# Kernel optimization log

Hardware: AMD Instinct MI355X
Metric: run time of the kernel (lower is better)

The kernel has to match this reference:

```python
import jax, jax.numpy as jnp
import numpy as np

N = 100000        # nodes
E_RAND = 1500000  # random edges (self loops appended -> E = 1.6M)
IN_DIM = 500
HID = 256
NCLASS = 50
K = 10


def setup_inputs() -> dict:
    key = jax.random.key(0)
    ks = jax.random.split(key, 8)
    feats = jax.random.normal(ks[0], (N, IN_DIM), dtype=jnp.float32)
    # edges: random + self loops (fit() adds self loops)
    src_r = jax.random.randint(ks[1], (E_RAND,), 0, N, dtype=jnp.int32)
    dst_r = jax.random.randint(ks[2], (E_RAND,), 0, N, dtype=jnp.int32)
    loop = jnp.arange(N, dtype=jnp.int32)
    src = jnp.concatenate([src_r, loop])
    dst = jnp.concatenate([dst_r, loop])
    # params (xavier-uniform-like scales)
    def xavier(k, shape):
        lim = np.sqrt(6.0 / (shape[0] + shape[1]))
        return jax.random.uniform(k, shape, jnp.float32, -lim, lim)
    W1 = xavier(ks[3], (IN_DIM, HID))
    b1 = jnp.zeros((HID,), jnp.float32)
    W2 = xavier(ks[4], (HID, NCLASS))
    b2 = jnp.zeros((NCLASS,), jnp.float32)
    s = xavier(ks[5], (NCLASS, 1))
    return {"feats": feats, "W1": W1, "b1": b1, "W2": W2, "b2": b2,
            "s": s, "src": src, "dst": dst}


def reference(feats, W1, b1, W2, b2, s, src, dst):
    # --- MLP (dropout is identity in eval / p=0) ---
    x = jax.nn.relu(feats @ W1 + b1)          # [N, HID]
    x = x @ W2 + b2                            # [N, NCLASS]
    # --- DAGNNConv: k-hop sym-normalized propagation ---
    deg = jax.ops.segment_sum(jnp.ones_like(dst, dtype=jnp.float32), dst,
                              num_segments=N)  # in-degrees
    norm = jnp.power(deg, -0.5)[:, None]       # [N, 1]
    results = [x]
    h = x
    for _ in range(K):
        h = h * norm
        h = jax.ops.segment_sum(h[src], dst, num_segments=N)  # copy_u + sum
        h = h * norm
        results.append(h)
    H = jnp.stack(results, axis=1)             # [N, K+1, C]
    S = jax.nn.sigmoid(jnp.einsum('nkc,co->nk', H, s))  # [N, K+1]
    out = jnp.einsum('nk,nkc->nc', S, H)       # [N, C]
    return out
```

## Files before the change

kernel.cpp:

```cpp
#include <hip/hip_runtime.h>
#include <hip/hip_bf16.h>
#include <math.h>

#define NN     100000
#define INDIM  500
#define HID    256
#define NCLASS 50
#define KHOPS  10
#define KPAD   512
#define CPAD   64

static inline size_t roundup256(size_t x) { return (x + 255) & ~(size_t)255; }

typedef __attribute__((ext_vector_type(8))) short bf16x8;
typedef __attribute__((ext_vector_type(4))) float f32x4;
typedef __attribute__((ext_vector_type(4))) short short4v;

__device__ inline short f2bf(float f) {
    union { float f; unsigned u; } v; v.f = f;
    unsigned r = v.u + 0x7FFFu + ((v.u >> 16) & 1u);
    return (short)(r >> 16);
}
__device__ inline float bflo(unsigned u) {
    union { unsigned u; float f; } v; v.u = u << 16; return v.f;
}
__device__ inline float bfhi(unsigned u) {
    union { unsigned u; float f; } v; v.u = u & 0xFFFF0000u; return v.f;
}
__device__ inline unsigned packbf(float a, float b) {
    return (unsigned)(unsigned short)f2bf(a) | ((unsigned)(unsigned short)f2bf(b) << 16);
}

__global__ void dagnn_zero2(int* __restrict__ a, int* __restrict__ b, int n) {
    int i = blockIdx.x * blockDim.x + threadIdx.x;
    if (i < n) { a[i] = 0; b[i] = 0; }
}

__global__ void dagnn_deg(const int* __restrict__ dst, int* __restrict__ degi, int E) {
    int e = blockIdx.x * blockDim.x + threadIdx.x;
    if (e < E) atomicAdd(&degi[dst[e]], 1);
}

__global__ void dagnn_norm(const int* __restrict__ degi, float* __restrict__ nrm, int n) {
    int i = blockIdx.x * blockDim.x + threadIdx.x;
    if (i < n) nrm[i] = rsqrtf((float)degi[i]);
}

__global__ void dagnn_scan(const int* __restrict__ degi, int* __restrict__ rowptr, int n) {
    __shared__ int wsum[16];
    __shared__ int carry_s;
    const int tid  = threadIdx.x;
    const int lane = tid & 63;
    const int wid  = tid >> 6;
    if (tid == 0) carry_s = 0;
    __syncthreads();
    for (int base = 0; base < n; base += 4096) {
        int i0 = base + tid * 4;
        int v0 = (i0 + 0 < n) ? degi[i0 + 0] : 0;
        int v1 = (i0 + 1 < n) ? degi[i0 + 1] : 0;
        int v2 = (i0 + 2 < n) ? degi[i0 + 2] : 0;
        int v3 = (i0 + 3 < n) ? degi[i0 + 3] : 0;
        int tsum = v0 + v1 + v2 + v3;
        int x = tsum;
        #pragma unroll
        for (int off = 1; off < 64; off <<= 1) {
            int t = __shfl_up(x, off);
            if (lane >= off) x += t;
        }
        if (lane == 63) wsum[wid] = x;
        __syncthreads();
        if (tid == 0) {
            int run = carry_s;
            #pragma unroll
            for (int w = 0; w < 16; ++w) { int t = wsum[w]; wsum[w] = run; run += t; }
            carry_s = run;
        }
        __syncthreads();
        int texcl = wsum[wid] + (x - tsum);
        if (i0 + 0 < n) rowptr[i0 + 0] = texcl;
        if (i0 + 1 < n) rowptr[i0 + 1] = texcl + v0;
        if (i0 + 2 < n) rowptr[i0 + 2] = texcl + v0 + v1;
        if (i0 + 3 < n) rowptr[i0 + 3] = texcl + v0 + v1 + v2;
        __syncthreads();
    }
    if (tid == 0) rowptr[n] = carry_s;
}

__global__ void dagnn_fill(const int* __restrict__ src, const int* __restrict__ dst,
                           const int* __restrict__ rowptr, int* __restrict__ fillc,
                           int* __restrict__ colidx, int E) {
    int e = blockIdx.x * blockDim.x + threadIdx.x;
    if (e >= E) return;
    int d = dst[e];
    int pos = rowptr[d] + atomicAdd(&fillc[d], 1);
    colidx[pos] = src[e];
}

__global__ void dagnn_w1t(const float* __restrict__ W1, short* __restrict__ W1t) {
    int idx = blockIdx.x * 256 + threadIdx.x;
    if (idx >= HID * KPAD) return;
    int n = idx >> 9;
    int k = idx & (KPAD - 1);
    float v = (k < INDIM) ? W1[(size_t)k * HID + n] : 0.f;
    W1t[idx] = f2bf(v);
}

__global__ void dagnn_w2t(const float* __restrict__ W2, short* __restrict__ W2t) {
    int idx = blockIdx.x * 256 + threadIdx.x;
    if (idx >= CPAD * HID) return;
    int n = idx >> 8;
    int k = idx & 255;
    float v = (n < NCLASS) ? W2[(size_t)k * NCLASS + n] : 0.f;
    W2t[idx] = f2bf(v);
}

__global__ void dagnn_sgate(const float* __restrict__ svec, float2* __restrict__ sg) {
    int c = threadIdx.x;
    if (c < 32) {
        float x = (2 * c     < NCLASS) ? svec[2 * c]     : 0.f;
        float y = (2 * c + 1 < NCLASS) ? svec[2 * c + 1] : 0.f;
        sg[c] = make_float2(x, y);
    }
}

#define G1_STRIDE 40
__global__ __launch_bounds__(512) void dagnn_gemm1_mfma(
        const float* __restrict__ A, const short* __restrict__ Bt,
        const float* __restrict__ bias, short* __restrict__ C, int M) {
    __shared__ __align__(16) short As[128 * G1_STRIDE];
    __shared__ __align__(16) short Bs[256 * G1_STRIDE];

    const int tid  = threadIdx.x;
    const int lane = tid & 63;
    const int wid  = tid >> 6;
    const int l16  = lane & 15;
    const int quad = lane >> 4;
    const int m_off = (wid & 1) * 64;
    const int n_off = (wid >> 1) * 64;
    const int row0  = blockIdx.x * 128;

    int am[2], aseg[2], bn[2], bseg[2];
    #pragma unroll
    for (int it = 0; it < 2; ++it) {
        int slot = tid + it * 512;
        am[it] = slot >> 3; aseg[it] = slot & 7;
        bn[it] = slot >> 2; bseg[it] = slot & 3;
    }

    float4 ra[2]; bf16x8 rb[2];

    #define LOAD_TILE(k0)                                                     \
        _Pragma("unroll")                                                     \
        for (int it = 0; it < 2; ++it) {                                      \
            int gm = row0 + am[it];                                           \
            int gk = (k0) + aseg[it] * 4;                                     \
            float4 f = {0.f, 0.f, 0.f, 0.f};                                  \
            if (gm < M) {                                                     \
                const float* ap = A + (size_t)gm * INDIM + gk;                \
                if (gk + 3 < INDIM) f = *(const float4*)ap;                   \
                else {                                                        \
                    if (gk + 0 < INDIM) f.x = ap[0];                          \
                    if (gk + 1 < INDIM) f.y = ap[1];                          \
                    if (gk + 2 < INDIM) f.z = ap[2];                          \
                    if (gk + 3 < INDIM) f.w = ap[3];                          \
                }                                                             \
            }                                                                 \
            ra[it] = f;                                                       \
            rb[it] = *(const bf16x8*)(Bt + (size_t)bn[it] * KPAD + (k0) + bseg[it] * 8); \
        }

    #define STORE_TILE()                                                      \
        _Pragma("unroll")                                                     \
        for (int it = 0; it < 2; ++it) {                                      \
            short4v sv;                                                       \
            sv.x = f2bf(ra[it].x); sv.y = f2bf(ra[it].y);                     \
            sv.z = f2bf(ra[it].z); sv.w = f2bf(ra[it].w);                     \
            *(short4v*)&As[am[it] * G1_STRIDE + aseg[it] * 4] = sv;           \
            *(bf16x8*)&Bs[bn[it] * G1_STRIDE + bseg[it] * 8] = rb[it];        \
        }

    f32x4 acc[4][4] = {};

    LOAD_TILE(0)
    STORE_TILE()
    __syncthreads();

    for (int ks = 0; ks < KPAD / 32; ++ks) {
        if (ks + 1 < KPAD / 32) { LOAD_TILE((ks + 1) * 32) }

        bf16x8 af[4], bfr[4];
        #pragma unroll
        for (int mt = 0; mt < 4; ++mt)
            af[mt] = *(const bf16x8*)&As[(m_off + mt * 16 + l16) * G1_STRIDE + quad * 8];
        #pragma unroll
        for (int nt = 0; nt < 4; ++nt)
            bfr[nt] = *(const bf16x8*)&Bs[(n_off + nt * 16 + l16) * G1_STRIDE + quad * 8];
        #pragma unroll
        for (int mt = 0; mt < 4; ++mt)
            #pragma unroll
            for (int nt = 0; nt < 4; ++nt)
                acc[mt][nt] = __builtin_amdgcn_mfma_f32_16x16x32_bf16(
                                  af[mt], bfr[nt], acc[mt][nt], 0, 0, 0);
        __syncthreads();
        if (ks + 1 < KPAD / 32) { STORE_TILE() }
        __syncthreads();
    }
    #undef LOAD_TILE
    #undef STORE_TILE

    #pragma unroll
    for (int nt = 0; nt < 4; ++nt) {
        int gc = n_off + nt * 16 + l16;
        float bb = bias[gc];
        #pragma unroll
        for (int mt = 0; mt < 4; ++mt) {
            #pragma unroll
            for (int r = 0; r < 4; ++r) {
                int gm = row0 + m_off + mt * 16 + quad * 4 + r;
                if (gm < M) {
                    float v = acc[mt][nt][r] + bb;
                    C[(size_t)gm * HID + gc] = f2bf(v > 0.f ? v : 0.f);
                }
            }
        }
    }
}

#define A2_STRIDE 72
#define B2_STRIDE 264
__global__ __launch_bounds__(256) void dagnn_mlp2_mfma(
        const short* __restrict__ hid, const short* __restrict__ W2t,
        const float* __restrict__ b2, const float* __restrict__ svec,
        const float* __restrict__ nrm,
        unsigned* __restrict__ hs0, float* __restrict__ out, int M) {
    __shared__ __align__(16) short As[128 * A2_STRIDE];
    __shared__ __align__(16) short Bs[CPAD * B2_STRIDE];

    const int tid  = threadIdx.x;
    const int lane = tid & 63;
    const int wid  = tid >> 6;
    const int l16  = lane & 15;
    const int quad = lane >> 4;
    const int m_off = wid * 32;
    const int row0  = blockIdx.x * 128;

    #pragma unroll
    for (int it = 0; it < 8; ++it) {
        int slot = tid + it * 256;
        int n   = slot >> 5;
        int seg = slot & 31;
        bf16x8 b = *(const bf16x8*)(W2t + (size_t)n * HID + seg * 8);
        *(bf16x8*)&Bs[n * B2_STRIDE + seg * 8] = b;
    }

    f32x4 acc[2][4] = {};

    for (int ks = 0; ks < HID / 64; ++ks) {
        const int k0 = ks * 64;
        #pragma unroll
        for (int it = 0; it < 4; ++it) {
            int slot = tid + it * 256;
            int m   = slot >> 3;
            int seg = slot & 7;
            int gm  = row0 + m;
            bf16x8 v = {};
            if (gm < M) v = *(const bf16x8*)(hid + (size_t)gm * HID + k0 + seg * 8);
            *(bf16x8*)&As[m * A2_STRIDE + seg * 8] = v;
        }
        __syncthreads();

        #pragma unroll
        for (int ksub = 0; ksub < 2; ++ksub) {
            bf16x8 af[2], bfr[4];
            #pragma unroll
            for (int mt = 0; mt < 2; ++mt)
                af[mt] = *(const bf16x8*)&As[(m_off + mt * 16 + l16) * A2_STRIDE
                                             + ksub * 32 + quad * 8];
            #pragma unroll
            for (int nt = 0; nt < 4; ++nt)
                bfr[nt] = *(const bf16x8*)&Bs[(nt * 16 + l16) * B2_STRIDE
                                              + k0 + ksub * 32 + quad * 8];
            #pragma unroll
            for (int mt = 0; mt < 2; ++mt)
                #pragma unroll
                for (int nt = 0; nt < 4; ++nt)
                    acc[mt][nt] = __builtin_amdgcn_mfma_f32_16x16x32_bf16(
                                      af[mt], bfr[nt], acc[mt][nt], 0, 0, 0);
        }
        __syncthreads();
    }

    float b2v[4], ssv[4];
    #pragma unroll
    for (int nt = 0; nt < 4; ++nt) {
        int gc = nt * 16 + l16;
        b2v[nt] = (gc < NCLASS) ? b2[gc]   : 0.f;
        ssv[nt] = (gc < NCLASS) ? svec[gc] : 0.f;
    }
    #pragma unroll
    for (int mt = 0; mt < 2; ++mt) {
        #pragma unroll
        for (int r = 0; r < 4; ++r) {
            int gm = row0 + m_off + mt * 16 + quad * 4 + r;
            float xv[4], q = 0.f;
            #pragma unroll
            for (int nt = 0; nt < 4; ++nt) {
                xv[nt] = acc[mt][nt][r] + b2v[nt];
                q += xv[nt] * ssv[nt];
            }
            #pragma unroll
            for (int off = 1; off < 16; off <<= 1) q += __shfl_xor(q, off);
            float S = 1.f / (1.f + __expf(-q));
            float nd = (gm < M) ? nrm[gm] : 0.f;
            #pragma unroll
            for (int nt = 0; nt < 4; ++nt) {
                int gc = nt * 16 + l16;
                float hv = xv[nt] * nd;
                float hp = __shfl_xor(hv, 1);
                if (gm < M) {
                    if (!(l16 & 1))
                        hs0[(size_t)gm * 32 + nt * 8 + (l16 >> 1)] = packbf(hv, hp);
                    if (gc < NCLASS) out[(size_t)gm * NCLASS + gc] = S * xv[nt];
                }
            }
        }
    }
}

__global__ __launch_bounds__(256) void dagnn_prop4(
        const unsigned* __restrict__ hs, const float* __restrict__ nrm,
        const int* __restrict__ rowptr, const int* __restrict__ colidx,
        const float2* __restrict__ sgate, unsigned* __restrict__ hs_next,
        float* __restrict__ out, int M, int write_next) {
    const int lane = threadIdx.x & 63;
    const int wid  = threadIdx.x >> 6;
    const int d    = blockIdx.x * 4 + wid;
    if (d >= M) return;
    const int half = lane >> 5;
    const int c    = lane & 31;
    const int beg = rowptr[d], end = rowptr[d + 1];

    float a0 = 0.f, a1 = 0.f;
    int e = beg;
    for (; e + 8 <= end; e += 8) {
        int s0 = colidx[e + half + 0];
        int s1 = colidx[e + half + 2];
        int s2 = colidx[e + half + 4];
        int s3 = colidx[e + half + 6];
        unsigned u0 = hs[(size_t)s0 * 32 + c];
        unsigned u1 = hs[(size_t)s1 * 32 + c];
        unsigned u2 = hs[(size_t)s2 * 32 + c];
        unsigned u3 = hs[(size_t)s3 * 32 + c];
        a0 += (bflo(u0) + bflo(u1)) + (bflo(u2) + bflo(u3));
        a1 += (bfhi(u0) + bfhi(u1)) + (bfhi(u2) + bfhi(u3));
    }
    for (; e + 2 <= end; e += 2) {
        int s = colidx[e + half];
        unsigned u = hs[(size_t)s * 32 + c];
        a0 += bflo(u); a1 += bfhi(u);
    }
    if (e < end && half == 0) {
        int s = colidx[e];
        unsigned u = hs[(size_t)s * 32 + c];
        a0 += bflo(u); a1 += bfhi(u);
    }
    a0 += __shfl_xor(a0, 32);
    a1 += __shfl_xor(a1, 32);

    float nd = nrm[d];
    float r0 = a0 * nd, r1 = a1 * nd;
    float2 g = sgate[c];
    float p = r0 * g.x + r1 * g.y;
    #pragma unroll
    for (int off = 16; off; off >>= 1) p += __shfl_xor(p, off);
    float S = 1.f / (1.f + __expf(-p));
    if (half == 0) {
        if (write_next) hs_next[(size_t)d * 32 + c] = packbf(r0 * nd, r1 * nd);
        int ch = 2 * c;
        if (ch < NCLASS) {
            out[(size_t)d * NCLASS + ch]     += S * r0;
            out[(size_t)d * NCLASS + ch + 1] += S * r1;
        }
    }
}

extern "C" void kernel_launch(void* const* d_in, const int* in_sizes, int n_in,
                              void* d_out, int out_size, void* d_ws, size_t ws_size,
                              hipStream_t stream) {
    const float* feats = (const float*)d_in[0];
    const float* W1    = (const float*)d_in[1];
    const float* b1    = (const float*)d_in[2];
    const float* W2    = (const float*)d_in[3];
    const float* b2    = (const float*)d_in[4];
    const float* svec  = (const float*)d_in[5];
    const int*   src   = (const int*)d_in[6];
    const int*   dst   = (const int*)d_in[7];
    float* out = (float*)d_out;

    const int M = in_sizes[0] / INDIM;
    const int E = in_sizes[6];

    char* p = (char*)d_ws;
    size_t off = 0;
    short*    hid   = (short*)   (p + off); off += roundup256((size_t)M * HID * 2);
    unsigned* hsA   = (unsigned*)(p + off); off += roundup256((size_t)M * 32 * 4);
    unsigned* hsB   = (unsigned*)(p + off); off += roundup256((size_t)M * 32 * 4);
    short*    W1t   = (short*)   (p + off); off += roundup256((size_t)HID * KPAD * 2);
    short*    W2t   = (short*)   (p + off); off += roundup256((size_t)CPAD * HID * 2);
    float2*   sgate = (float2*)  (p + off); off += roundup256(32 * sizeof(float2));
    int*      degi  = (int*)     (p + off); off += roundup256((size_t)M * 4);
    float*    nrm   = (float*)   (p + off); off += roundup256((size_t)M * 4);
    int*      rowptr= (int*)     (p + off); off += roundup256((size_t)(M + 1) * 4);
    int*      fillc = (int*)     (p + off); off += roundup256((size_t)M * 4);
    int*      colidx= (int*)     (p + off); off += roundup256((size_t)E * 4);
    (void)ws_size;

    dagnn_zero2<<<(M + 255) / 256, 256, 0, stream>>>(degi, fillc, M);
    dagnn_deg<<<(E + 255) / 256, 256, 0, stream>>>(dst, degi, E);
    dagnn_norm<<<(M + 255) / 256, 256, 0, stream>>>(degi, nrm, M);
    dagnn_scan<<<1, 1024, 0, stream>>>(degi, rowptr, M);
    dagnn_fill<<<(E + 255) / 256, 256, 0, stream>>>(src, dst, rowptr, fillc, colidx, E);

    dagnn_w1t<<<(HID * KPAD + 255) / 256, 256, 0, stream>>>(W1, W1t);
    dagnn_w2t<<<(CPAD * HID + 255) / 256, 256, 0, stream>>>(W2, W2t);
    dagnn_sgate<<<1, 32, 0, stream>>>(svec, sgate);

    dagnn_gemm1_mfma<<<(M + 127) / 128, 512, 0, stream>>>(feats, W1t, b1, hid, M);
    dagnn_mlp2_mfma<<<(M + 127) / 128, 256, 0, stream>>>(hid, W2t, b2, svec, nrm,
                                                         hsA, out, M);

    unsigned* hin = hsA;
    unsigned* hout = hsB;
    for (int k = 0; k < KHOPS; ++k) {
        dagnn_prop4<<<(M + 3) / 4, 256, 0, stream>>>(hin, nrm, rowptr, colidx,
                                                     sgate, hout, out, M,
                                                     k < KHOPS - 1);
        unsigned* t = hin; hin = hout; hout = t;
    }
}
```

Measured before the change: 1.176 ms.

## Split GEMM1 columns across blocks and widen propagation gathers to 4 classes per lane

The first GEMM now launches a 2D grid where each 256-thread block computes a 128x128 output tile instead of one 512-thread block covering all 256 columns. This halves the LDS footprint per block and doubles the block count, but each block re-reads and re-converts the same fp32 feature rows. The propagation kernel now has 16 lanes each gather 4 bf16 classes (uint2) with 4 edges in flight per wave instead of 2. It also uses clamped indices instead of separate tail loops, and vectorizes the output and next-hop stores.

```diff
diff --git a/kernel.cpp b/kernel.cpp
--- a/kernel.cpp
+++ b/kernel.cpp
@@ -114,21 +114,24 @@
     W2t[idx] = f2bf(v);
 }
 
-__global__ void dagnn_sgate(const float* __restrict__ svec, float2* __restrict__ sg) {
-    int c = threadIdx.x;
-    if (c < 32) {
-        float x = (2 * c     < NCLASS) ? svec[2 * c]     : 0.f;
-        float y = (2 * c + 1 < NCLASS) ? svec[2 * c + 1] : 0.f;
-        sg[c] = make_float2(x, y);
+__global__ void dagnn_sgate4(const float* __restrict__ svec, float4* __restrict__ sg) {
+    int q = threadIdx.x;
+    if (q < 16) {
+        float4 g;
+        g.x = (4 * q + 0 < NCLASS) ? svec[4 * q + 0] : 0.f;
+        g.y = (4 * q + 1 < NCLASS) ? svec[4 * q + 1] : 0.f;
+        g.z = (4 * q + 2 < NCLASS) ? svec[4 * q + 2] : 0.f;
+        g.w = (4 * q + 3 < NCLASS) ? svec[4 * q + 3] : 0.f;
+        sg[q] = g;
     }
 }
 
 #define G1_STRIDE 40
-__global__ __launch_bounds__(512) void dagnn_gemm1_mfma(
+__global__ __launch_bounds__(256) void dagnn_gemm1_mfma(
         const float* __restrict__ A, const short* __restrict__ Bt,
         const float* __restrict__ bias, short* __restrict__ C, int M) {
     __shared__ __align__(16) short As[128 * G1_STRIDE];
-    __shared__ __align__(16) short Bs[256 * G1_STRIDE];
+    __shared__ __align__(16) short Bs[128 * G1_STRIDE];
 
     const int tid  = threadIdx.x;
     const int lane = tid & 63;
@@ -138,20 +141,25 @@
     const int m_off = (wid & 1) * 64;
     const int n_off = (wid >> 1) * 64;
     const int row0  = blockIdx.x * 128;
-
-    int am[2], aseg[2], bn[2], bseg[2];
+    const int col0  = blockIdx.y * 128;
+
+    int am[4], aseg[4], bn[2], bseg[2];
+    #pragma unroll
+    for (int it = 0; it < 4; ++it) {
+        int slot = tid + it * 256;
+        am[it] = slot >> 3; aseg[it] = slot & 7;
+    }
     #pragma unroll
     for (int it = 0; it < 2; ++it) {
-        int slot = tid + it * 512;
-        am[it] = slot >> 3; aseg[it] = slot & 7;
+        int slot = tid + it * 256;
         bn[it] = slot >> 2; bseg[it] = slot & 3;
     }
 
-    float4 ra[2]; bf16x8 rb[2];
+    float4 ra[4]; bf16x8 rb[2];
 
     #define LOAD_TILE(k0)                                                     \
         _Pragma("unroll")                                                     \
-        for (int it = 0; it < 2; ++it) {                                      \
+        for (int it = 0; it < 4; ++it) {                                      \
             int gm = row0 + am[it];                                           \
             int gk = (k0) + aseg[it] * 4;                                     \
             float4 f = {0.f, 0.f, 0.f, 0.f};                                  \
@@ -166,18 +174,23 @@
                 }                                                             \
             }                                                                 \
             ra[it] = f;                                                       \
-            rb[it] = *(const bf16x8*)(Bt + (size_t)bn[it] * KPAD + (k0) + bseg[it] * 8); \
-        }
+        }                                                                     \
+        _Pragma("unroll")                                                     \
+        for (int it = 0; it < 2; ++it)                                        \
+            rb[it] = *(const bf16x8*)(Bt + (size_t)(col0 + bn[it]) * KPAD     \
+                                      + (k0) + bseg[it] * 8);
 
     #define STORE_TILE()                                                      \
         _Pragma("unroll")                                                     \
-        for (int it = 0; it < 2; ++it) {                                      \
+        for (int it = 0; it < 4; ++it) {                                      \
             short4v sv;                                                       \
             sv.x = f2bf(ra[it].x); sv.y = f2bf(ra[it].y);                     \
             sv.z = f2bf(ra[it].z); sv.w = f2bf(ra[it].w);                     \
             *(short4v*)&As[am[it] * G1_STRIDE + aseg[it] * 4] = sv;           \
-            *(bf16x8*)&Bs[bn[it] * G1_STRIDE + bseg[it] * 8] = rb[it];        \
-        }
+        }                                                                     \
+        _Pragma("unroll")                                                     \
+        for (int it = 0; it < 2; ++it)                                        \
+            *(bf16x8*)&Bs[bn[it] * G1_STRIDE + bseg[it] * 8] = rb[it];
 
     f32x4 acc[4][4] = {};
 
@@ -210,7 +223,7 @@
 
     #pragma unroll
     for (int nt = 0; nt < 4; ++nt) {
-        int gc = n_off + nt * 16 + l16;
+        int gc = col0 + n_off + nt * 16 + l16;
         float bb = bias[gc];
         #pragma unroll
         for (int mt = 0; mt < 4; ++mt) {
@@ -327,59 +340,67 @@
     }
 }
 
-__global__ __launch_bounds__(256) void dagnn_prop4(
+__global__ __launch_bounds__(256) void dagnn_prop5(
         const unsigned* __restrict__ hs, const float* __restrict__ nrm,
         const int* __restrict__ rowptr, const int* __restrict__ colidx,
-        const float2* __restrict__ sgate, unsigned* __restrict__ hs_next,
+        const float4* __restrict__ sg4, unsigned* __restrict__ hs_next,
         float* __restrict__ out, int M, int write_next) {
     const int lane = threadIdx.x & 63;
     const int wid  = threadIdx.x >> 6;
     const int d    = blockIdx.x * 4 + wid;
     if (d >= M) return;
-    const int half = lane >> 5;
-    const int c    = lane & 31;
+    const int sub = lane >> 4;
+    const int q   = lane & 15;
     const int beg = rowptr[d], end = rowptr[d + 1];
 
-    float a0 = 0.f, a1 = 0.f;
-    int e = beg;
-    for (; e + 8 <= end; e += 8) {
-        int s0 = colidx[e + half + 0];
-        int s1 = colidx[e + half + 2];
-        int s2 = colidx[e + half + 4];
-        int s3 = colidx[e + half + 6];
-        unsigned u0 = hs[(size_t)s0 * 32 + c];
-        unsigned u1 = hs[(size_t)s1 * 32 + c];
-        unsigned u2 = hs[(size_t)s2 * 32 + c];
-        unsigned u3 = hs[(size_t)s3 * 32 + c];
-        a0 += (bflo(u0) + bflo(u1)) + (bflo(u2) + bflo(u3));
-        a1 += (bfhi(u0) + bfhi(u1)) + (bfhi(u2) + bfhi(u3));
-    }
-    for (; e + 2 <= end; e += 2) {
-        int s = colidx[e + half];
-        unsigned u = hs[(size_t)s * 32 + c];
-        a0 += bflo(u); a1 += bfhi(u);
-    }
-    if (e < end && half == 0) {
-        int s = colidx[e];
-        unsigned u = hs[(size_t)s * 32 + c];
-        a0 += bflo(u); a1 += bfhi(u);
-    }
-    a0 += __shfl_xor(a0, 32);
-    a1 += __shfl_xor(a1, 32);
+    float a0 = 0.f, a1 = 0.f, a2 = 0.f, a3 = 0.f;
+    for (int e = beg; e < end; e += 8) {
+        int i0 = e + sub;
+        int i1 = e + 4 + sub;
+        int s0 = colidx[(i0 < end) ? i0 : (end - 1)];
+        int s1 = colidx[(i1 < end) ? i1 : (end - 1)];
+        uint2 u0 = *(const uint2*)&hs[(size_t)s0 * 32 + q * 2];
+        uint2 u1 = *(const uint2*)&hs[(size_t)s1 * 32 + q * 2];
+        if (i0 < end) {
+            a0 += bflo(u0.x); a1 += bfhi(u0.x);
+            a2 += bflo(u0.y); a3 += bfhi(u0.y);
+        }
+        if (i1 < end) {
+            a0 += bflo(u1.x); a1 += bfhi(u1.x);
+            a2 += bflo(u1.y); a3 += bfhi(u1.y);
+        }
+    }
+    a0 += __shfl_xor(a0, 16); a0 += __shfl_xor(a0, 32);
+    a1 += __shfl_xor(a1, 16); a1 += __shfl_xor(a1, 32);
+    a2 += __shfl_xor(a2, 16); a2 += __shfl_xor(a2, 32);
+    a3 += __shfl_xor(a3, 16); a3 += __shfl_xor(a3, 32);
 
     float nd = nrm[d];
-    float r0 = a0 * nd, r1 = a1 * nd;
-    float2 g = sgate[c];
-    float p = r0 * g.x + r1 * g.y;
-    #pragma unroll
-    for (int off = 16; off; off >>= 1) p += __shfl_xor(p, off);
+    float r0 = a0 * nd, r1 = a1 * nd, r2 = a2 * nd, r3 = a3 * nd;
+    float4 g = sg4[q];
+    float p = r0 * g.x + r1 * g.y + r2 * g.z + r3 * g.w;
+    #pragma unroll
+    for (int off = 1; off < 16; off <<= 1) p += __shfl_xor(p, off);
     float S = 1.f / (1.f + __expf(-p));
-    if (half == 0) {
-        if (write_next) hs_next[(size_t)d * 32 + c] = packbf(r0 * nd, r1 * nd);
-        int ch = 2 * c;
-        if (ch < NCLASS) {
-            out[(size_t)d * NCLASS + ch]     += S * r0;
-            out[(size_t)d * NCLASS + ch + 1] += S * r1;
+
+    if (sub == 0) {
+        if (write_next) {
+            uint2 w;
+            w.x = packbf(r0 * nd, r1 * nd);
+            w.y = packbf(r2 * nd, r3 * nd);
+            *(uint2*)&hs_next[(size_t)d * 32 + q * 2] = w;
+        }
+        int ch = 4 * q;
+        float* op = out + (size_t)d * NCLASS + ch;
+        if (ch + 1 < NCLASS) {
+            float2 o = *(float2*)op;
+            o.x += S * r0; o.y += S * r1;
+            *(float2*)op = o;
+        }
+        if (ch + 3 < NCLASS) {
+            float2 o = *(float2*)(op + 2);
+            o.x += S * r2; o.y += S * r3;
+            *(float2*)(op + 2) = o;
         }
     }
 }
@@ -407,7 +428,7 @@
     unsigned* hsB   = (unsigned*)(p + off); off += roundup256((size_t)M * 32 * 4);
     short*    W1t   = (short*)   (p + off); off += roundup256((size_t)HID * KPAD * 2);
     short*    W2t   = (short*)   (p + off); off += roundup256((size_t)CPAD * HID * 2);
-    float2*   sgate = (float2*)  (p + off); off += roundup256(32 * sizeof(float2));
+    float4*   sg4   = (float4*)  (p + off); off += roundup256(16 * sizeof(float4));
     int*      degi  = (int*)     (p + off); off += roundup256((size_t)M * 4);
     float*    nrm   = (float*)   (p + off); off += roundup256((size_t)M * 4);
     int*      rowptr= (int*)     (p + off); off += roundup256((size_t)(M + 1) * 4);
@@ -423,17 +444,18 @@
 
     dagnn_w1t<<<(HID * KPAD + 255) / 256, 256, 0, stream>>>(W1, W1t);
     dagnn_w2t<<<(CPAD * HID + 255) / 256, 256, 0, stream>>>(W2, W2t);
-    dagnn_sgate<<<1, 32, 0, stream>>>(svec, sgate);
-
-    dagnn_gemm1_mfma<<<(M + 127) / 128, 512, 0, stream>>>(feats, W1t, b1, hid, M);
+    dagnn_sgate4<<<1, 64, 0, stream>>>(svec, sg4);
+
+    dim3 g1((M + 127) / 128, 2);
+    dagnn_gemm1_mfma<<<g1, 256, 0, stream>>>(feats, W1t, b1, hid, M);
     dagnn_mlp2_mfma<<<(M + 127) / 128, 256, 0, stream>>>(hid, W2t, b2, svec, nrm,
                                                          hsA, out, M);
 
     unsigned* hin = hsA;
     unsigned* hout = hsB;
     for (int k = 0; k < KHOPS; ++k) {
-        dagnn_prop4<<<(M + 3) / 4, 256, 0, stream>>>(hin, nrm, rowptr, colidx,
-                                                     sgate, hout, out, M,
+        dagnn_prop5<<<(M + 3) / 4, 256, 0, stream>>>(hin, nrm, rowptr, colidx,
+                                                     sg4, hout, out, M,
                                                      k < KHOPS - 1);
         unsigned* t = hin; hin = hout; hout = t;
     }
```

Result: slower. 1.274 ms (+8.4%).
